# Performance work log

Hardware: AMD Instinct MI355X
Metric: run time of the kernel (lower is better)

The kernel has to match this reference:

```python
import jax, jax.numpy as jnp
import numpy as np

S_PADDING = 65
T_PADDING = 65


def setup_inputs() -> dict:
    key = jax.random.key(0)
    k1, k2 = jax.random.split(key)
    s = jax.random.normal(k1, (32, 16, 64, 63), dtype=jnp.float32)
    t = jax.random.normal(k2, (32, 16, 64, 63), dtype=jnp.float32)
    return {"s": s, "t": t}


def reference(s, t):
    # s, t: [B, N, L, D] real. Original stacks a zero imaginary part,
    # zero-pads the D dim (dim 3 of the 5D tensor), FFTs along it,
    # then for each shift i rolls fs along N, complex-multiplies with ft,
    # concatenates along N, IFFTs, keeps real part, and permutes to [B, N*N, Dp, L].
    B, N, L, D = s.shape
    s_pad = jnp.pad(s, ((0, 0), (0, 0), (0, 0), (0, S_PADDING)))  # [B,N,L,Dp]
    t_pad = jnp.pad(t, ((0, 0), (0, 0), (0, 0), (0, T_PADDING)))
    FS = jnp.fft.fft(s_pad, axis=-1)  # complex64 [B,N,L,Dp]
    FT = jnp.fft.fft(t_pad, axis=-1)
    # roll(fs, i, axis=1)[:, n] == fs[:, (n - i) % N]; loop i is outer in the cat
    idx = (jnp.arange(N)[None, :] - jnp.arange(N)[:, None]) % N  # [i, n]
    FS_all = FS[:, idx]  # [B, N(i), N(n), L, Dp]
    Hf = FS_all * FT[:, None]  # broadcast over shift dim i
    Dp = D + S_PADDING
    Hf = Hf.reshape(B, N * N, L, Dp)
    H = jnp.fft.ifft(Hf, axis=-1).real  # [B, N*N, L, Dp]
    return H.transpose(0, 1, 3, 2)  # [B, N*N, Dp, L]
```

## Files before the change

kernel.cpp:

```cpp
#include <hip/hip_runtime.h>


#define D_IN 63
#define L_DIM 64
#define N_DIM 16
#define DP 128
#define B_DIM 32

__global__ __launch_bounds__(256) void transpose_kernel(
    const float* __restrict__ s, const float* __restrict__ t,
    float* __restrict__ so, float* __restrict__ to)
{
    const int tile = blockIdx.x;
    const int bn   = tile & (B_DIM * N_DIM - 1);
    const float* __restrict__ src =
        (tile < B_DIM * N_DIM ? s : t) + (size_t)bn * (L_DIM * D_IN);
    float* __restrict__ dst =
        (tile < B_DIM * N_DIM ? so : to) + (size_t)bn * (L_DIM * D_IN);

    __shared__ float lds[L_DIM * D_IN];

    for (int f = threadIdx.x; f < L_DIM * D_IN; f += 256)
        lds[f] = src[f];
    __syncthreads();

    for (int g = threadIdx.x; g < L_DIM * D_IN; g += 256) {
        const int d = g >> 6;
        const int l = g & 63;
        dst[g] = lds[l * D_IN + d];
    }
}

__global__ __launch_bounds__(64) void conv_kernel_t(
    const float* __restrict__ st, const float* __restrict__ tt,
    float* __restrict__ out)
{
    const int blk = blockIdx.x;
    const int b  = blk >> 8;
    const int ij = blk & 255;
    const int i  = ij >> 4;
    const int j  = ij & 15;
    const int k  = (j - i) & 15;
    const int l  = threadIdx.x;

    const float* __restrict__ srow = st + (((size_t)b * N_DIM + k) * D_IN) * L_DIM + l;
    const float* __restrict__ trow = tt + (((size_t)b * N_DIM + j) * D_IN) * L_DIM + l;

    float sv[D_IN], tv[D_IN];
#pragma unroll
    for (int c = 0; c < D_IN; ++c) sv[c] = srow[(size_t)c * L_DIM];
#pragma unroll
    for (int c = 0; c < D_IN; ++c) tv[c] = trow[(size_t)c * L_DIM];

    __shared__ float xpose[16 * 65];

    float* __restrict__ obase = out + ((size_t)blk * (DP * L_DIM));

    const int rq = l >> 4;
    const int c4 = (l & 15) << 2;

#pragma unroll
    for (int d0 = 0; d0 < DP; d0 += 16) {
        float acc[16];
#pragma unroll
        for (int dd = 0; dd < 16; ++dd) acc[dd] = 0.0f;

#pragma unroll
        for (int ks = 0; ks < D_IN; ++ks) {
#pragma unroll
            for (int dd = 0; dd < 16; ++dd) {
                const int kt = d0 + dd - ks;
                if (kt >= 0 && kt < D_IN)
                    acc[dd] += sv[ks] * tv[kt];
            }
        }

#pragma unroll
        for (int dd = 0; dd < 16; ++dd)
            xpose[dd * 65 + l] = acc[dd];

#pragma unroll
        for (int q = 0; q < 4; ++q) {
            const int r = (q << 2) + rq;
            const float4 v = *reinterpret_cast<const float4*>(&xpose[r * 65 + c4]);
            *reinterpret_cast<float4*>(&obase[(size_t)(d0 + r) * L_DIM + c4]) = v;
        }
    }
}

__global__ __launch_bounds__(64) void conv_kernel_fallback(
    const float* __restrict__ s, const float* __restrict__ t,
    float* __restrict__ out)
{
    const int blk = blockIdx.x;
    const int b  = blk >> 8;
    const int ij = blk & 255;
    const int i  = ij >> 4;
    const int j  = ij & 15;
    const int k  = (j - i) & 15;
    const int l  = threadIdx.x;

    const float* __restrict__ srow = s + ((((size_t)b * N_DIM + k) * L_DIM + l) * D_IN);
    const float* __restrict__ trow = t + ((((size_t)b * N_DIM + j) * L_DIM + l) * D_IN);

    float sv[D_IN], tv[D_IN];
#pragma unroll
    for (int c = 0; c < D_IN; ++c) sv[c] = srow[c];
#pragma unroll
    for (int c = 0; c < D_IN; ++c) tv[c] = trow[c];

    float* __restrict__ orow = out + ((size_t)blk * (DP * L_DIM)) + l;

#pragma unroll
    for (int d0 = 0; d0 < DP; d0 += 16) {
        float acc[16];
#pragma unroll
        for (int dd = 0; dd < 16; ++dd) acc[dd] = 0.0f;
#pragma unroll
        for (int ks = 0; ks < D_IN; ++ks) {
#pragma unroll
            for (int dd = 0; dd < 16; ++dd) {
                const int kt = d0 + dd - ks;
                if (kt >= 0 && kt < D_IN)
                    acc[dd] += sv[ks] * tv[kt];
            }
        }
#pragma unroll
        for (int dd = 0; dd < 16; ++dd)
            orow[(size_t)(d0 + dd) * L_DIM] = acc[dd];
    }
}

extern "C" void kernel_launch(void* const* d_in, const int* in_sizes, int n_in,
                              void* d_out, int out_size, void* d_ws, size_t ws_size,
                              hipStream_t stream) {
    const float* s = (const float*)d_in[0];
    const float* t = (const float*)d_in[1];
    float* out = (float*)d_out;

    const size_t elems = (size_t)B_DIM * N_DIM * L_DIM * D_IN;
    const size_t need  = 2 * elems * sizeof(float);

    if (d_ws != nullptr && ws_size >= need) {
        float* so = (float*)d_ws;
        float* to = so + elems;
        hipLaunchKernelGGL(transpose_kernel, dim3(2 * B_DIM * N_DIM), dim3(256), 0, stream,
                           s, t, so, to);
        hipLaunchKernelGGL(conv_kernel_t, dim3(B_DIM * N_DIM * N_DIM), dim3(64), 0, stream,
                           so, to, out);
    } else {
        hipLaunchKernelGGL(conv_kernel_fallback, dim3(B_DIM * N_DIM * N_DIM), dim3(64), 0, stream,
                           s, t, out);
    }
}
```

Measured before the change: 294.8 us.

## Share t row in LDS across eight shifts per block and loop over kt

The convolution kernel now launches 512-thread blocks that each handle one (b, j) pair and eight shift values i. The t row is loaded once into shared memory and reused by all eight waves, instead of every 64-thread block reloading it into registers. The inner loop now iterates over t indices read from LDS, with sv kept in registers. This cuts register pressure and global traffic for t, at the cost of an LDS read per kt step and a larger block-wide sync and LDS footprint.

Result: slower. 350.5 us (+18.9%).

```diff
diff --git a/kernel.cpp b/kernel.cpp
--- a/kernel.cpp
+++ b/kernel.cpp
@@ -31,30 +31,41 @@
     }
 }
 
-__global__ __launch_bounds__(64) void conv_kernel_t(
+__global__ __launch_bounds__(512, 4) void conv_kernel_t2(
     const float* __restrict__ st, const float* __restrict__ tt,
     float* __restrict__ out)
 {
-    const int blk = blockIdx.x;
-    const int b  = blk >> 8;
-    const int ij = blk & 255;
-    const int i  = ij >> 4;
-    const int j  = ij & 15;
-    const int k  = (j - i) & 15;
-    const int l  = threadIdx.x;
+    const int bi   = blockIdx.x;
+    const int half = bi & 1;
+    const int j    = (bi >> 1) & 15;
+    const int b    = bi >> 5;
+    const int wid  = threadIdx.x >> 6;
+    const int l    = threadIdx.x & 63;
+    const int i    = half * 8 + wid;
+    const int k    = (j - i) & 15;
 
-    const float* __restrict__ srow = st + (((size_t)b * N_DIM + k) * D_IN) * L_DIM + l;
-    const float* __restrict__ trow = tt + (((size_t)b * N_DIM + j) * D_IN) * L_DIM + l;
+    __shared__ float tvt[D_IN * L_DIM];
+    __shared__ float xp[8][8 * 68];
 
-    float sv[D_IN], tv[D_IN];
+    {
+        const float* __restrict__ trow = tt + ((size_t)(b * N_DIM + j) * D_IN) * L_DIM;
+#pragma unroll
+        for (int it = 0; it < 8; ++it) {
+            const int f = it * 512 + (int)threadIdx.x;
+            if (f < D_IN * L_DIM) tvt[f] = trow[f];
+        }
+    }
+
+    const float* __restrict__ srow = st + ((size_t)(b * N_DIM + k) * D_IN) * L_DIM + l;
+    float sv[D_IN];
 #pragma unroll
     for (int c = 0; c < D_IN; ++c) sv[c] = srow[(size_t)c * L_DIM];
-#pragma unroll
-    for (int c = 0; c < D_IN; ++c) tv[c] = trow[(size_t)c * L_DIM];
 
-    __shared__ float xpose[16 * 65];
+    __syncthreads();
 
+    const int blk = ((b * N_DIM + i) * N_DIM + j);
     float* __restrict__ obase = out + ((size_t)blk * (DP * L_DIM));
+    float* __restrict__ xw = &xp[wid][0];
 
     const int rq = l >> 4;
     const int c4 = (l & 15) << 2;
@@ -65,25 +76,31 @@
 #pragma unroll
         for (int dd = 0; dd < 16; ++dd) acc[dd] = 0.0f;
 
+        const int kt_lo = (d0 - 62 < 0) ? 0 : (d0 - 62);
+        const int kt_hi = (d0 + 15 > 62) ? 62 : (d0 + 15);
 #pragma unroll
-        for (int ks = 0; ks < D_IN; ++ks) {
+        for (int kt = kt_lo; kt <= kt_hi; ++kt) {
+            const float v = tvt[kt * L_DIM + l];
 #pragma unroll
             for (int dd = 0; dd < 16; ++dd) {
-                const int kt = d0 + dd - ks;
-                if (kt >= 0 && kt < D_IN)
-                    acc[dd] += sv[ks] * tv[kt];
+                const int ks = d0 + dd - kt;
+                if (ks >= 0 && ks < D_IN)
+                    acc[dd] += sv[ks] * v;
             }
         }
 
 #pragma unroll
-        for (int dd = 0; dd < 16; ++dd)
-            xpose[dd * 65 + l] = acc[dd];
-
+        for (int g = 0; g < 2; ++g) {
 #pragma unroll
-        for (int q = 0; q < 4; ++q) {
-            const int r = (q << 2) + rq;
-            const float4 v = *reinterpret_cast<const float4*>(&xpose[r * 65 + c4]);
-            *reinterpret_cast<float4*>(&obase[(size_t)(d0 + r) * L_DIM + c4]) = v;
+            for (int r = 0; r < 8; ++r)
+                xw[r * 68 + l] = acc[g * 8 + r];
+#pragma unroll
+            for (int q = 0; q < 2; ++q) {
+                const int r_ = rq + (q << 2);
+                const float4 v4 = *reinterpret_cast<const float4*>(&xw[r_ * 68 + c4]);
+                *reinterpret_cast<float4*>(
+                    &obase[(size_t)(d0 + g * 8 + r_) * L_DIM + c4]) = v4;
+            }
         }
     }
 }
@@ -146,7 +163,7 @@
         float* to = so + elems;
         hipLaunchKernelGGL(transpose_kernel, dim3(2 * B_DIM * N_DIM), dim3(256), 0, stream,
                            s, t, so, to);
-        hipLaunchKernelGGL(conv_kernel_t, dim3(B_DIM * N_DIM * N_DIM), dim3(64), 0, stream,
+        hipLaunchKernelGGL(conv_kernel_t2, dim3(B_DIM * N_DIM * 2), dim3(512), 0, stream,
                            so, to, out);
     } else {
         hipLaunchKernelGGL(conv_kernel_fallback, dim3(B_DIM * N_DIM * N_DIM), dim3(64), 0, stream,
```
